# Kernel tuning notes

Measured on AMD Instinct MI355X. Metric: run time of the kernel, lower is better.

## Reference

```python
import jax, jax.numpy as jnp
import numpy as np

T, N, E, D = 6, 50000, 250000, 256   # edge types, nodes/type, edges/type, feat dim
H, C, K = 4, 64, 64                  # heads, head dim, diffpool clusters (H*C == D)
SCALE = 0.06


def setup_inputs():
    key = jax.random.key(0)
    ks = jax.random.split(key, 14)
    return {
        'x_pkg': jax.random.normal(ks[0], (N, D), jnp.float32),
        'x_dst': jax.random.normal(ks[1], (T, N, D), jnp.float32),
        'edge_index': jax.random.randint(ks[2], (T, 2, E), 0, N, jnp.int32),
        'edge_attr': jax.random.uniform(ks[3], (T, E, 1), jnp.float32),
        'node_mask': jnp.ones((N,), jnp.float32),
        'edge_mask': jax.random.uniform(ks[4], (E,), jnp.float32),
        'W1_src': jax.random.normal(ks[5], (T, D, H, C), jnp.float32) * SCALE,
        'W1_dst': jax.random.normal(ks[6], (T, D, H, C), jnp.float32) * SCALE,
        'a1': jax.random.normal(ks[7], (T, H, C), jnp.float32) * SCALE,
        'W2_src': jax.random.normal(ks[8], (T, D, H, C), jnp.float32) * SCALE,
        'W2_dst': jax.random.normal(ks[9], (T, D, H, C), jnp.float32) * SCALE,
        'a2': jax.random.normal(ks[10], (T, H, C), jnp.float32) * SCALE,
        'W_assign': jax.random.normal(ks[11], (D, K), jnp.float32) * SCALE,
        'W_cls': jax.random.normal(ks[12], (D + T, 1), jnp.float32) * SCALE,
        'b_cls': jnp.zeros((1,), jnp.float32),
    }


def _gatv2(x_src, x_dst, src, dst, Ws, Wd, a, edge_w):
    """GATv2Conv (bipartite, no self loops) with soft edge-mask weighting."""
    hs = jnp.einsum('nd,dhc->nhc', x_src, Ws)          # [N,H,C]
    hd = jnp.einsum('nd,dhc->nhc', x_dst, Wd)          # [N,H,C]
    hj = hs[src]                                        # [E,H,C] gathered source msgs
    e = jnp.sum(a * jax.nn.leaky_relu(hd[dst] + hj, 0.2), axis=-1)  # [E,H]
    m = jax.ops.segment_max(e, dst, num_segments=N)
    m = jnp.where(jnp.isfinite(m), m, 0.0)              # nodes with no in-edges
    p = jnp.exp(e - m[dst])
    den = jax.ops.segment_sum(p, dst, num_segments=N)
    alpha = p / (den[dst] + 1e-16)                      # softmax over in-neighbors
    msg = (alpha * edge_w[:, None])[:, :, None] * hj    # [E,H,C]
    return jax.ops.segment_sum(msg, dst, num_segments=N).reshape(N, H * C)


def reference(x_pkg, x_dst, edge_index, edge_attr, node_mask, edge_mask,
              W1_src, W1_dst, a1, W2_src, W2_dst, a2, W_assign, W_cls, b_cls):
    nm = node_mask[:, None]
    xm_pkg = x_pkg * nm
    # layer 1: hetero GATv2 per edge type (Package_Name -> dst type)
    h1 = [
        _gatv2(xm_pkg, x_dst[t] * nm, edge_index[t, 0], edge_index[t, 1],
               W1_src[t], W1_dst[t], a1[t], edge_mask)
        for t in range(T)
    ]
    # layer 2 on relu'd features (H*C == D so dims line up)
    x2_src = jax.nn.relu(x_pkg)
    h2 = [
        _gatv2(x2_src, jax.nn.relu(h1[t]), edge_index[t, 0], edge_index[t, 1],
               W2_src[t], W2_dst[t], a2[t], edge_mask)
        for t in range(T)
    ]
    # diffpool on last processed node type
    x_last = h2[-1]                                     # [N, D]
    S = jax.nn.softmax(x_last @ W_assign, axis=-1)      # [N, K] cluster assignment
    x_pool = S.T @ x_last                               # [K, D]
    # global aggregated edge features (mean per edge type)
    agg_edge = jnp.concatenate([edge_attr[t].mean(axis=0) for t in range(T)], -1)  # [T]
    feats = jnp.concatenate([x_pool, jnp.broadcast_to(agg_edge, (K, T))], axis=-1)
    logits = feats @ W_cls + b_cls                      # [K, 1]
    return jax.nn.sigmoid(logits)
```

## Files before the change

### kernel.cpp

```cpp
#include <hip/hip_runtime.h>
#include <math.h>

#define NN 50000
#define EE 250000
#define TTT 6
#define DD 256
#define HH 4
#define CC 64
#define KDIM 64

typedef __bf16 bf16x4 __attribute__((ext_vector_type(4)));
typedef __bf16 bf16x8 __attribute__((ext_vector_type(8)));
typedef float  f32x4  __attribute__((ext_vector_type(4)));

__device__ __forceinline__ void mfma_bf16(f32x4& d, bf16x8 a, bf16x8 b) {
    asm("v_mfma_f32_16x16x32_bf16 %0, %1, %2, %0" : "+v"(d) : "v"(a), "v"(b));
}

__global__ __launch_bounds__(256) void prep_b_k(
    const float* __restrict__ B0, const float* __restrict__ B1,
    const float* __restrict__ B2, const float* __restrict__ B3,
    __bf16* __restrict__ outp)
{
    int w = blockIdx.y;
    const float* B = (w == 0) ? B0 : (w == 1) ? B1 : (w == 2) ? B2 : B3;
    __bf16* oh = outp + (size_t)w * 2 * DD * DD;
    __bf16* ol = oh + DD * DD;
    int i = blockIdx.x * 256 + threadIdx.x;
    int k = i >> 8, n = i & 255;
    float x = B[i];
    __bf16 h = (__bf16)x;
    __bf16 l = (__bf16)(x - (float)h);
    oh[(size_t)n * DD + k] = h;
    ol[(size_t)n * DD + k] = l;
}

#define BM 128
#define BN 128
#define BK 64

__global__ __launch_bounds__(256, 2) void gemm_mfma_k(
    const float* __restrict__ A, const __bf16* __restrict__ Bt,
    float* __restrict__ Cout, const float* __restrict__ rowscale,
    int op, int nrows)
{
    __shared__ __align__(16) __bf16 Ah[BM * BK], Al[BM * BK];
    __shared__ __align__(16) __bf16 Bh[BN * BK], Bl[BN * BK];
    const __bf16* Bth = Bt;
    const __bf16* Btl = Bt + DD * DD;
    int tid = threadIdx.x;
    int row0 = blockIdx.x * BM;
    int col0 = blockIdx.y * BN;
    int lane = tid & 63;
    int wv = tid >> 6;
    int wm = (wv >> 1) * 64;
    int wn = (wv & 1) * 64;
    f32x4 acc[4][4] = {};

    for (int k0 = 0; k0 < DD; k0 += BK) {
        #pragma unroll
        for (int li = 0; li < 8; ++li) {
            int i = tid + li * 256;
            int r = i >> 4;
            int kq = (i & 15) * 4;
            int gr = row0 + r;
            float4 v = make_float4(0.f, 0.f, 0.f, 0.f);
            if (gr < nrows) {
                v = *(const float4*)&A[(size_t)gr * DD + k0 + kq];
                if (op == 0) {
                    float s = rowscale[gr];
                    v.x *= s; v.y *= s; v.z *= s; v.w *= s;
                } else {
                    v.x = fmaxf(v.x, 0.f); v.y = fmaxf(v.y, 0.f);
                    v.z = fmaxf(v.z, 0.f); v.w = fmaxf(v.w, 0.f);
                }
            }
            bf16x4 hv, lv;
            hv[0] = (__bf16)v.x; hv[1] = (__bf16)v.y;
            hv[2] = (__bf16)v.z; hv[3] = (__bf16)v.w;
            lv[0] = (__bf16)(v.x - (float)hv[0]);
            lv[1] = (__bf16)(v.y - (float)hv[1]);
            lv[2] = (__bf16)(v.z - (float)hv[2]);
            lv[3] = (__bf16)(v.w - (float)hv[3]);
            int kk = kq ^ ((r & 7) << 3);
            *(bf16x4*)&Ah[r * BK + kk] = hv;
            *(bf16x4*)&Al[r * BK + kk] = lv;
        }
        #pragma unroll
        for (int li = 0; li < 4; ++li) {
            int i = tid + li * 256;
            int r = i >> 3;
            int kc = (i & 7) * 8;
            int kk = kc ^ ((r & 7) << 3);
            *(bf16x8*)&Bh[r * BK + kk] = *(const bf16x8*)&Bth[(size_t)(col0 + r) * DD + k0 + kc];
            *(bf16x8*)&Bl[r * BK + kk] = *(const bf16x8*)&Btl[(size_t)(col0 + r) * DD + k0 + kc];
        }
        __syncthreads();
        #pragma unroll
        for (int ks = 0; ks < 2; ++ks) {
            bf16x8 af[4], alf[4], bfr[4], blf[4];
            int kb = ks * 32 + (lane >> 4) * 8;
            #pragma unroll
            for (int i2 = 0; i2 < 4; ++i2) {
                int r = wm + i2 * 16 + (lane & 15);
                int kk = kb ^ ((r & 7) << 3);
                af[i2]  = *(const bf16x8*)&Ah[r * BK + kk];
                alf[i2] = *(const bf16x8*)&Al[r * BK + kk];
            }
            #pragma unroll
            for (int j = 0; j < 4; ++j) {
                int r = wn + j * 16 + (lane & 15);
                int kk = kb ^ ((r & 7) << 3);
                bfr[j] = *(const bf16x8*)&Bh[r * BK + kk];
                blf[j] = *(const bf16x8*)&Bl[r * BK + kk];
            }
            #pragma unroll
            for (int i2 = 0; i2 < 4; ++i2)
                #pragma unroll
                for (int j = 0; j < 4; ++j) {
                    mfma_bf16(acc[i2][j], af[i2],  bfr[j]);
                    mfma_bf16(acc[i2][j], af[i2],  blf[j]);
                    mfma_bf16(acc[i2][j], alf[i2], bfr[j]);
                }
        }
        __syncthreads();
    }
    #pragma unroll
    for (int i2 = 0; i2 < 4; ++i2) {
        int rbase = row0 + wm + i2 * 16 + (lane >> 4) * 4;
        #pragma unroll
        for (int rr = 0; rr < 4; ++rr) {
            int gr = rbase + rr;
            if (gr < nrows) {
                #pragma unroll
                for (int j = 0; j < 4; ++j)
                    Cout[(size_t)gr * DD + col0 + wn + j * 16 + (lane & 15)] = acc[i2][j][rr];
            }
        }
    }
}

__global__ __launch_bounds__(256) void count_k(const int* __restrict__ dst,
                                               int* __restrict__ deg, int nedges)
{
    int e = blockIdx.x * 256 + threadIdx.x;
    if (e < nedges) atomicAdd(&deg[dst[e]], 1);
}

__global__ __launch_bounds__(1024) void scan_k(const int* __restrict__ deg,
                                               int* __restrict__ offs)
{
    __shared__ int part[1024];
    int tid = threadIdx.x;
    const int CH = (NN + 1023) / 1024;
    int base = tid * CH;
    int s = 0;
    for (int i = 0; i < CH; ++i)
        if (base + i < NN) s += deg[base + i];
    part[tid] = s;
    __syncthreads();
    for (int off = 1; off < 1024; off <<= 1) {
        int v = (tid >= off) ? part[tid - off] : 0;
        __syncthreads();
        part[tid] += v;
        __syncthreads();
    }
    int run = part[tid] - s;
    for (int i = 0; i < CH; ++i) {
        if (base + i < NN) { offs[base + i] = run; run += deg[base + i]; }
    }
    if (tid == 1023) offs[NN] = part[1023];
}

__global__ __launch_bounds__(256) void scatter_k(const int* __restrict__ dst,
                                                 const int* __restrict__ offs,
                                                 int* __restrict__ cursor,
                                                 int* __restrict__ eord, int nedges)
{
    int e = blockIdx.x * 256 + threadIdx.x;
    if (e < nedges) {
        int d = dst[e];
        int p = atomicAdd(&cursor[d], 1);
        eord[offs[d] + p] = e;
    }
}

__global__ __launch_bounds__(256) void edge_fused_k(
    const float* __restrict__ hs, const float* __restrict__ hd,
    const int* __restrict__ src, const float* __restrict__ emask,
    const int* __restrict__ eord, const int* __restrict__ offs,
    const float* __restrict__ avec, float* __restrict__ hout)
{
    int lane = threadIdx.x & 63;
    int n = (int)((blockIdx.x * 256 + threadIdx.x) >> 6);
    if (n >= NN) return;
    float hdv[HH], av[HH], den[HH], accv[HH];
    #pragma unroll
    for (int h = 0; h < HH; ++h) {
        hdv[h] = hd[(size_t)n * DD + h * CC + lane];
        av[h] = avec[h * CC + lane];
        den[h] = 0.f; accv[h] = 0.f;
    }
    int b = offs[n], e2 = offs[n + 1];
    for (int idx = b; idx < e2; ++idx) {
        int e = eord[idx];
        int s = src[e];
        float ew = emask[e];
        const float* prs = hs + (size_t)s * DD;
        #pragma unroll
        for (int h = 0; h < HH; ++h) {
            float hsv = prs[h * CC + lane];
            float xx = hdv[h] + hsv;
            xx = xx > 0.f ? xx : 0.2f * xx;
            float v = av[h] * xx;
            #pragma unroll
            for (int off = 32; off; off >>= 1) v += __shfl_xor(v, off, 64);
            float p = expf(v);
            den[h] += p;
            accv[h] = fmaf(p * ew, hsv, accv[h]);
        }
    }
    #pragma unroll
    for (int h = 0; h < HH; ++h)
        hout[(size_t)n * DD + h * CC + lane] = accv[h] / (den[h] + 1e-16f);
}

#define MBLK 120
__global__ __launch_bounds__(256) void edge_mean1_k(
    const float* __restrict__ eattr, double* __restrict__ partial, int nedges)
{
    __shared__ double sh[256];
    int tid = threadIdx.x;
    int stride = MBLK * 256;
    #pragma unroll
    for (int t = 0; t < TTT; ++t) {
        double a = 0.0;
        for (int i = blockIdx.x * 256 + tid; i < nedges; i += stride)
            a += (double)eattr[(size_t)t * nedges + i];
        sh[tid] = a;
        __syncthreads();
        #pragma unroll
        for (int s = 128; s; s >>= 1) {
            if (tid < s) sh[tid] += sh[tid + s];
            __syncthreads();
        }
        if (tid == 0) partial[(size_t)blockIdx.x * TTT + t] = sh[0];
        __syncthreads();
    }
}

#define AM 64
#define AK 32
__global__ __launch_bounds__(256) void assign_reduce_k(
    const float* __restrict__ x, const float* __restrict__ Wa,
    const float* __restrict__ wcls, float* __restrict__ logit_acc, int nrows)
{
    __shared__ __align__(16) float As[AK][AM + 4];
    __shared__ __align__(16) float Bs[AK][KDIM];
    __shared__ float wc[DD];
    __shared__ float Ps[AM][KDIM + 1];
    __shared__ float zp[4][AM];
    __shared__ float zsh[AM], rs[AM];
    int tid = threadIdx.x;
    int row0 = blockIdx.x * AM;
    int tx = tid & 15, ty = tid >> 4;
    for (int i = tid; i < DD; i += 256) wc[i] = wcls[i];
    float acc[4][4] = {};
    float zacc = 0.f;
    int node = tid & 63, part = tid >> 6;
    for (int k0 = 0; k0 < DD; k0 += AK) {
        for (int i = tid; i < AM * AK; i += 256) {
            int r = i / AK, k = i % AK;
            int gr = row0 + r;
            As[k][r] = (gr < nrows) ? x[(size_t)gr * DD + k0 + k] : 0.f;
        }
        for (int i = tid; i < AK * KDIM; i += 256) {
            int k = i >> 6, m = i & 63;
            Bs[k][m] = Wa[(size_t)(k0 + k) * KDIM + m];
        }
        __syncthreads();
        #pragma unroll
        for (int kk = 0; kk < AK; ++kk) {
            float4 a4 = *(const float4*)&As[kk][ty * 4];
            float4 b4 = *(const float4*)&Bs[kk][tx * 4];
            float av[4] = {a4.x, a4.y, a4.z, a4.w};
            float bv[4] = {b4.x, b4.y, b4.z, b4.w};
            #pragma unroll
            for (int i2 = 0; i2 < 4; ++i2)
                #pragma unroll
                for (int j = 0; j < 4; ++j)
                    acc[i2][j] = fmaf(av[i2], bv[j], acc[i2][j]);
        }
        #pragma unroll
        for (int kk = part * 8; kk < part * 8 + 8; ++kk)
            zacc = fmaf(As[kk][node], wc[k0 + kk], zacc);
        __syncthreads();
    }
    #pragma unroll
    for (int i2 = 0; i2 < 4; ++i2)
        #pragma unroll
        for (int j = 0; j < 4; ++j)
            Ps[ty * 4 + i2][tx * 4 + j] = acc[i2][j];
    zp[part][node] = zacc;
    __syncthreads();
    if (tid < AM) {
        float z = zp[0][tid] + zp[1][tid] + zp[2][tid] + zp[3][tid];
        zsh[tid] = z;
        float m = -1e30f;
        for (int k = 0; k < KDIM; ++k) m = fmaxf(m, Ps[tid][k]);
        float s = 0.f;
        for (int k = 0; k < KDIM; ++k) {
            float v = expf(Ps[tid][k] - m);
            Ps[tid][k] = v;
            s += v;
        }
        rs[tid] = s;
    }
    __syncthreads();
    if (tid < KDIM) {
        float t = 0.f;
        for (int n = 0; n < AM; ++n)
            t += Ps[n][tid] / rs[n] * zsh[n];
        atomicAdd(&logit_acc[tid], t);
    }
}

__global__ void final_k(const float* __restrict__ logit, const double* __restrict__ partial,
                        const float* __restrict__ Wcls, const float* __restrict__ bcls,
                        float* __restrict__ out)
{
    int k = threadIdx.x;
    double acc = (double)logit[k];
    #pragma unroll
    for (int t = 0; t < TTT; ++t) {
        double s = 0.0;
        for (int b = 0; b < MBLK; ++b) s += partial[(size_t)b * TTT + t];
        acc += (s / (double)EE) * (double)Wcls[DD + t];
    }
    acc += (double)bcls[0];
    out[k] = (float)(1.0 / (1.0 + exp(-acc)));
}

extern "C" void kernel_launch(void* const* d_in, const int* in_sizes, int n_in,
                              void* d_out, int out_size, void* d_ws, size_t ws_size,
                              hipStream_t stream)
{
    const float* x_pkg   = (const float*)d_in[0];
    const float* x_dst   = (const float*)d_in[1];
    const int*   eindex  = (const int*)d_in[2];
    const float* eattr   = (const float*)d_in[3];
    const float* nmask   = (const float*)d_in[4];
    const float* emask   = (const float*)d_in[5];
    const float* W1s     = (const float*)d_in[6];
    const float* W1d     = (const float*)d_in[7];
    const float* a1      = (const float*)d_in[8];
    const float* W2s     = (const float*)d_in[9];
    const float* W2d     = (const float*)d_in[10];
    const float* a2      = (const float*)d_in[11];
    const float* Wassign = (const float*)d_in[12];
    const float* Wcls    = (const float*)d_in[13];
    const float* bcls    = (const float*)d_in[14];
    float* out = (float*)d_out;

    const int t = TTT - 1;
    const int* src5 = eindex + (size_t)t * 2 * EE;
    const int* dst5 = src5 + EE;
    const float* xdst5 = x_dst + (size_t)t * NN * DD;
    const float* W1s5 = W1s + (size_t)t * DD * HH * CC;
    const float* W1d5 = W1d + (size_t)t * DD * HH * CC;
    const float* a15  = a1 + (size_t)t * HH * CC;
    const float* W2s5 = W2s + (size_t)t * DD * HH * CC;
    const float* W2d5 = W2d + (size_t)t * DD * HH * CC;
    const float* a25  = a2 + (size_t)t * HH * CC;

    char* wsb = (char*)d_ws;
    size_t off = 0;
    auto carve = [&](size_t bytes) -> void* {
        void* p = wsb + off;
        off += (bytes + 255) & ~(size_t)255;
        return p;
    };
    float* hs     = (float*)carve((size_t)NN * DD * sizeof(float));
    float* hd     = (float*)carve((size_t)NN * DD * sizeof(float));
    float* hbuf   = (float*)carve((size_t)NN * DD * sizeof(float));
    int*   deg    = (int*)carve((size_t)NN * sizeof(int));
    int*   cursor = (int*)carve((size_t)NN * sizeof(int));
    int*   offs   = (int*)carve((size_t)(NN + 1) * sizeof(int));
    int*   eord   = (int*)carve((size_t)EE * sizeof(int));
    float* logit  = (float*)carve(KDIM * sizeof(float));
    double* partial = (double*)carve((size_t)MBLK * TTT * sizeof(double));
    __bf16* bprep = (__bf16*)carve((size_t)4 * 2 * DD * DD * sizeof(__bf16));

    dim3 ggrid((NN + BM - 1) / BM, DD / BN);
    int edge_node_blocks = (NN + 3) / 4;
    int eb = (EE + 255) / 256;

    hipMemsetAsync(deg, 0, (size_t)NN * sizeof(int), stream);
    hipMemsetAsync(cursor, 0, (size_t)NN * sizeof(int), stream);
    hipMemsetAsync(logit, 0, KDIM * sizeof(float), stream);

    prep_b_k<<<dim3(256, 4), 256, 0, stream>>>(W1s5, W1d5, W2s5, W2d5, bprep);
    edge_mean1_k<<<MBLK, 256, 0, stream>>>(eattr, partial, EE);
    count_k<<<eb, 256, 0, stream>>>(dst5, deg, EE);
    scan_k<<<1, 1024, 0, stream>>>(deg, offs);
    scatter_k<<<eb, 256, 0, stream>>>(dst5, offs, cursor, eord, EE);

    gemm_mfma_k<<<ggrid, 256, 0, stream>>>(x_pkg, bprep + 0 * 2 * DD * DD, hs, nmask, 0, NN);
    gemm_mfma_k<<<ggrid, 256, 0, stream>>>(xdst5, bprep + 1 * 2 * DD * DD, hd, nmask, 0, NN);
    edge_fused_k<<<edge_node_blocks, 256, 0, stream>>>(hs, hd, src5, emask, eord, offs, a15, hbuf);

    gemm_mfma_k<<<ggrid, 256, 0, stream>>>(hbuf, bprep + 3 * 2 * DD * DD, hd, nullptr, 1, NN);
    gemm_mfma_k<<<ggrid, 256, 0, stream>>>(x_pkg, bprep + 2 * 2 * DD * DD, hs, nullptr, 1, NN);
    edge_fused_k<<<edge_node_blocks, 256, 0, stream>>>(hs, hd, src5, emask, eord, offs, a25, hbuf);

    assign_reduce_k<<<(NN + AM - 1) / AM, 256, 0, stream>>>(hbuf, Wassign, Wcls, logit, NN);
    final_k<<<1, KDIM, 0, stream>>>(logit, partial, Wcls, bcls, out);
}
```

Before: 993.0 us.

## Process four edges per wavefront in GATv2 edge kernel with float4 loads

```diff
diff --git a/kernel.cpp b/kernel.cpp
--- a/kernel.cpp
+++ b/kernel.cpp
@@ -194,35 +194,72 @@
     int lane = threadIdx.x & 63;
     int n = (int)((blockIdx.x * 256 + threadIdx.x) >> 6);
     if (n >= NN) return;
-    float hdv[HH], av[HH], den[HH], accv[HH];
+    int eslot = lane >> 4;
+    int c16 = lane & 15;
+    float hdv[HH][4], av[HH][4], accv[HH][4], den[HH];
     #pragma unroll
     for (int h = 0; h < HH; ++h) {
-        hdv[h] = hd[(size_t)n * DD + h * CC + lane];
-        av[h] = avec[h * CC + lane];
-        den[h] = 0.f; accv[h] = 0.f;
+        float4 t = *(const float4*)&hd[(size_t)n * DD + h * CC + c16 * 4];
+        hdv[h][0] = t.x; hdv[h][1] = t.y; hdv[h][2] = t.z; hdv[h][3] = t.w;
+        float4 u = *(const float4*)&avec[h * CC + c16 * 4];
+        av[h][0] = u.x; av[h][1] = u.y; av[h][2] = u.z; av[h][3] = u.w;
+        accv[h][0] = accv[h][1] = accv[h][2] = accv[h][3] = 0.f;
+        den[h] = 0.f;
     }
     int b = offs[n], e2 = offs[n + 1];
-    for (int idx = b; idx < e2; ++idx) {
-        int e = eord[idx];
+    for (int i0 = b; i0 < e2; i0 += 4) {
+        int idx = i0 + eslot;
+        bool valid = idx < e2;
+        int idxc = valid ? idx : b;
+        int e = eord[idxc];
         int s = src[e];
         float ew = emask[e];
         const float* prs = hs + (size_t)s * DD;
+        float hsv[HH][4], v[HH];
         #pragma unroll
         for (int h = 0; h < HH; ++h) {
-            float hsv = prs[h * CC + lane];
-            float xx = hdv[h] + hsv;
-            xx = xx > 0.f ? xx : 0.2f * xx;
-            float v = av[h] * xx;
-            #pragma unroll
-            for (int off = 32; off; off >>= 1) v += __shfl_xor(v, off, 64);
-            float p = expf(v);
-            den[h] += p;
-            accv[h] = fmaf(p * ew, hsv, accv[h]);
-        }
-    }
-    #pragma unroll
-    for (int h = 0; h < HH; ++h)
-        hout[(size_t)n * DD + h * CC + lane] = accv[h] / (den[h] + 1e-16f);
+            float4 t = *(const float4*)&prs[h * CC + c16 * 4];
+            hsv[h][0] = t.x; hsv[h][1] = t.y; hsv[h][2] = t.z; hsv[h][3] = t.w;
+            float vv = 0.f;
+            #pragma unroll
+            for (int j = 0; j < 4; ++j) {
+                float xx = hdv[h][j] + hsv[h][j];
+                xx = xx > 0.f ? xx : 0.2f * xx;
+                vv = fmaf(av[h][j], xx, vv);
+            }
+            v[h] = vv;
+        }
+        #pragma unroll
+        for (int h = 0; h < HH; ++h) {
+            float vv = v[h];
+            #pragma unroll
+            for (int off = 1; off < 16; off <<= 1) vv += __shfl_xor(vv, off, 64);
+            float pf = valid ? expf(vv) : 0.f;
+            den[h] += pf;
+            float pw = pf * ew;
+            #pragma unroll
+            for (int j = 0; j < 4; ++j)
+                accv[h][j] = fmaf(pw, hsv[h][j], accv[h][j]);
+        }
+    }
+    #pragma unroll
+    for (int h = 0; h < HH; ++h) {
+        den[h] += __shfl_xor(den[h], 16, 64);
+        den[h] += __shfl_xor(den[h], 32, 64);
+        #pragma unroll
+        for (int j = 0; j < 4; ++j) {
+            accv[h][j] += __shfl_xor(accv[h][j], 16, 64);
+            accv[h][j] += __shfl_xor(accv[h][j], 32, 64);
+        }
+    }
+    if (eslot == 0) {
+        #pragma unroll
+        for (int h = 0; h < HH; ++h) {
+            float r = 1.f / (den[h] + 1e-16f);
+            float4 o = { accv[h][0] * r, accv[h][1] * r, accv[h][2] * r, accv[h][3] * r };
+            *(float4*)&hout[(size_t)n * DD + h * CC + c16 * 4] = o;
+        }
+    }
 }
 
 #define MBLK 120
```

After: 964.4 us. -2.9%, faster.
